# Kernel optimization log

Measured on AMD Instinct MI355X. Metric: run time of the kernel, lower is better.

## Reference

```python
import jax, jax.numpy as jnp
import numpy as np


def setup_inputs() -> dict:
    key = jax.random.key(0)
    k1, k2, k3 = jax.random.split(key, 3)
    B, D, F, P = 4096, 1024, 2048, 1024
    return {
        "x": jax.random.normal(k1, (B, D), dtype=jnp.float32),
        "features": jax.random.normal(k2, (F, D), dtype=jnp.float32),
        "prototypes": jax.random.normal(k3, (P, D), dtype=jnp.float32),
        "alpha": jnp.ones((1,), dtype=jnp.float32),
        "beta": jnp.ones((1,), dtype=jnp.float32),
        "theta": jnp.ones((1,), dtype=jnp.float32),
    }


def reference(x, features, prototypes, alpha, beta, theta):
    # Project each set ONCE (the original redundantly broadcasts first).
    xf = x @ features.T            # [B, F]
    pf = prototypes @ features.T   # [P, F]
    sx = jax.nn.sigmoid(xf)        # x_present [B, F]
    sp = jax.nn.sigmoid(pf)        # p_present [P, F]
    ax = xf * sx                   # [B, F]
    bp = pf * sp                   # [P, F]
    # common[b,p]        = sum_f xf*pf*sx*sp            = (xf*sx) @ (pf*sp)^T
    # x_distinct[b,p]    = sum_f xf*sx*(1-sp)           = rowsum(xf*sx) - (xf*sx) @ sp^T
    # p_distinct[b,p]    = sum_f pf*sp*(1-sx)           = rowsum(pf*sp) - sx @ (pf*sp)^T
    common = ax @ bp.T                                     # [B, P]
    x_distinctive = ax.sum(axis=1, keepdims=True) - ax @ sp.T  # [B, P]
    p_distinctive = bp.sum(axis=1)[None, :] - sx @ bp.T        # [B, P]
    return theta * common - alpha * x_distinctive - beta * p_distinctive
```

## Files before the change

### kernel.cpp

```cpp
#include <hip/hip_runtime.h>
#include <hip/hip_bf16.h>

typedef __bf16 bf16_t;
typedef bf16_t bf16x4 __attribute__((ext_vector_type(4)));
typedef bf16_t bf16x8 __attribute__((ext_vector_type(8)));
typedef float f32x4 __attribute__((ext_vector_type(4)));

#define AS1 __attribute__((address_space(1)))
#define AS3 __attribute__((address_space(3)))

__device__ __forceinline__ void gload_lds16(const void* g, void* l) {
    __builtin_amdgcn_global_load_lds((const AS1 void*)g, (AS3 void*)l, 16, 0, 0);
}
__device__ __forceinline__ void gload_lds4(const void* g, void* l) {
    __builtin_amdgcn_global_load_lds((const AS1 void*)g, (AS3 void*)l, 4, 0, 0);
}

__device__ __forceinline__ float sigmoidf_(float v) {
    return 1.0f / (1.0f + __expf(-v));
}

__global__ __launch_bounds__(256) void k_convert3(const float* __restrict__ x,
                                                  const float* __restrict__ pr,
                                                  const float* __restrict__ ft,
                                                  bf16_t* __restrict__ XPs,
                                                  bf16_t* __restrict__ F16s) {
    const int n4 = 7168 * 256;
    int i = blockIdx.x * 256 + threadIdx.x;
    const int stride = gridDim.x * 256;
    for (; i < n4; i += stride) {
        float4 v;
        long r;
        int c4;
        bf16_t* dst;
        long R;
        if (i < 1048576) {
            v = ((const float4*)x)[i];
            r = i >> 8; c4 = i & 255; dst = XPs; R = 5120;
        } else if (i < 1310720) {
            const int j = i - 1048576;
            v = ((const float4*)pr)[j];
            r = 4096 + (j >> 8); c4 = j & 255; dst = XPs; R = 5120;
        } else {
            const int j = i - 1310720;
            v = ((const float4*)ft)[j];
            r = j >> 8; c4 = j & 255; dst = F16s; R = 2048;
        }
        const int col = c4 << 2;
        const int kb = col >> 5;
        const int cw = col & 31;
        bf16x4 o;
        o[0] = (bf16_t)v.x; o[1] = (bf16_t)v.y; o[2] = (bf16_t)v.z; o[3] = (bf16_t)v.w;
        *(bf16x4*)(dst + ((long)kb * R + r) * 32 + cw) = o;
    }
}

__global__ __launch_bounds__(256) void k_foldrs(const float* __restrict__ rsPart,
                                                float* __restrict__ rsums) {
    const int r = blockIdx.x * 256 + threadIdx.x;
    float s = 0.f;
#pragma unroll
    for (int b = 0; b < 8; ++b) s += rsPart[b * 5120 + r];
    rsums[r] = s;
}

__global__ __launch_bounds__(256) void k_reduce4(const bf16_t* __restrict__ part,
                                                 const float* __restrict__ rsums,
                                                 const float* __restrict__ pa,
                                                 float* __restrict__ out) {
    const int idx = blockIdx.x * 256 + threadIdx.x;
    const int region = idx >> 13;
    const int widx = idx & 8191;
    const int wv = widx >> 10;
    const int chunk = (widx >> 6) & 15;
    const int ln = widx & 63;
    const int bx = region >> 2, by = region & 3;
    const int wm = wv >> 2, wn = wv & 3;
    const int fg = chunk >> 1, gp = chunk & 1;
    const int er = (ln >> 4) << 2, ec = ln & 15;
    const long off = (long)idx * 8;

    float sum[8] = {};
#pragma unroll
    for (int s = 0; s < 4; ++s) {
        bf16x8 v = *(const bf16x8*)(part + (long)s * 4194304 + off);
#pragma unroll
        for (int j = 0; j < 8; ++j) sum[j] += (float)v[j];
    }
    const int r0 = bx * 256 + wm * 128 + fg * 16 + er;
    const int c0 = by * 256 + wn * 64 + gp * 32 + ec;
    const float a = pa[0];
#pragma unroll
    for (int q = 0; q < 4; ++q) {
        const float ra = a * rsums[r0 + q];
#pragma unroll
        for (int gh = 0; gh < 2; ++gh) {
            const int c = c0 + gh * 16;
            out[(long)(r0 + q) * 1024 + c] = sum[gh * 4 + q] - ra - rsums[4096 + c];
        }
    }
}

__global__ __launch_bounds__(512, 2) void gemm2_8p(
    const bf16_t* __restrict__ A2s, const bf16_t* __restrict__ B2s,
    bf16_t* __restrict__ O1, long zstride) {
    __shared__ char lds[131072];
    const int tid = threadIdx.x;
    const int wave = tid >> 6, lane = tid & 63;
    const int wm = wave >> 2, wn = wave & 3;

    const int gx = gridDim.x, gy = gridDim.y;
    const int o = blockIdx.x + gx * (blockIdx.y + gy * blockIdx.z);
    const int cpx = (gx * gy * (int)gridDim.z) >> 3;
    const int v = (o & 7) * cpx + (o >> 3);
    const int bx = v % gx;
    const int rem = v / gx;
    const int by = rem % gy;
    const int bz = rem / gy;

    const long bm = (long)bx * 256, bn = (long)by * 256;
    const int kb32_0 = bz * 32;
    const char* Ab = (const char*)A2s;
    const char* Bb = (const char*)B2s;

    const int swzcb = ((lane >> 4) << 4) ^ (((lane >> 3) & 1) << 5);
    const int base_a = (wm * 128 + (lane & 15)) * 64 + swzcb;
    const int base_b = (wn * 64 + (lane & 15)) * 64 + swzcb;

    f32x4 acc[8][4] = {};

    auto STAGEC = [&](const char* gbase, int ldsoff) {
#pragma unroll
        for (int j = 0; j < 2; ++j) {
            const int oo = (j * 512 + tid) << 4;
            const int cb = (oo & 63) ^ (((oo >> 9) & 1) << 5);
            gload_lds16(gbase + (oo & ~63) + cb, lds + ldsoff + (oo & ~1023));
        }
    };

#define VM8 asm volatile("s_waitcnt vmcnt(8)" ::: "memory")
#define VM4 asm volatile("s_waitcnt vmcnt(4)" ::: "memory")
#define VM0 asm volatile("s_waitcnt vmcnt(0)" ::: "memory")

    auto PFETCH = [&](int pf) {
        const long kb = kb32_0 + pf;
        const int ps = pf & 3;
        STAGEC(Ab + (kb * 4096 + bm) * 64, ps * 16384);
        STAGEC(Bb + (kb * 1024 + bn) * 64, 65536 + ps * 16384);
    };

#define PHASE2(p, WAITSTMT, DOPF)                                               \
    do {                                                                        \
        WAITSTMT;                                                               \
        __builtin_amdgcn_s_barrier();                                           \
        __builtin_amdgcn_s_setprio(1);                                          \
        const int slot = (p) & 3;                                               \
        const char* sA = lds + slot * 16384;                                    \
        const char* sB = lds + 65536 + slot * 16384;                            \
        bf16x8 af[8];                                                           \
        bf16x8 bfr[4];                                                          \
        _Pragma("unroll") for (int f = 0; f < 8; ++f)                           \
            af[f] = *(const bf16x8*)(sA + base_a + f * 1024);                   \
        _Pragma("unroll") for (int g = 0; g < 4; ++g)                           \
            bfr[g] = *(const bf16x8*)(sB + base_b + g * 1024);                  \
        if (DOPF) PFETCH((p) + 3);                                              \
        _Pragma("unroll") for (int f = 0; f < 8; ++f)                           \
            _Pragma("unroll") for (int g = 0; g < 4; ++g)                       \
                acc[f][g] = __builtin_amdgcn_mfma_f32_16x16x32_bf16(            \
                    af[f], bfr[g], acc[f][g], 0, 0, 0);                         \
        __builtin_amdgcn_s_setprio(0);                                          \
    } while (0)

    const int NP = 32;
    PFETCH(0);
    PFETCH(1);
    PFETCH(2);

    for (int p = 0; p < NP - 3; ++p) PHASE2(p, VM8, 1);
    PHASE2(NP - 3, VM8, 0);
    PHASE2(NP - 2, VM4, 0);
    PHASE2(NP - 1, VM0, 0);

#undef PHASE2
#undef VM8
#undef VM4
#undef VM0

    bf16_t* Op = O1 + (long)bz * zstride + (long)(bx * 4 + by) * 65536 +
                 wave * 8192 + lane * 8;
#pragma unroll
    for (int fg = 0; fg < 8; ++fg)
#pragma unroll
        for (int gp = 0; gp < 2; ++gp) {
            bf16x8 w;
#pragma unroll
            for (int gh = 0; gh < 2; ++gh)
#pragma unroll
                for (int q = 0; q < 4; ++q)
                    w[gh * 4 + q] = (bf16_t)acc[fg][gp * 2 + gh][q];
            *(bf16x8*)(Op + (fg * 2 + gp) * 512) = w;
        }
}

__global__ __launch_bounds__(512, 2) void gemm1_160(
    const bf16_t* __restrict__ XPs, const bf16_t* __restrict__ F16s,
    bf16_t* __restrict__ A2s, bf16_t* __restrict__ B2s,
    float* __restrict__ rsPart,
    const float* __restrict__ pa, const float* __restrict__ pb,
    const float* __restrict__ pt) {
    __shared__ char lds[106496];
    const int tid = threadIdx.x;
    const int wave = tid >> 6, lane = tid & 63;
    const int wm = wave >> 2, wn = wave & 3;

    const int gx = gridDim.x, gy = gridDim.y;
    const int o = blockIdx.x + gx * blockIdx.y;
    const int cpx = (gx * gy) >> 3;
    const int v = (o & 7) * cpx + (o >> 3);
    const int bx = v % gx;
    const int by = v / gx;

    const long bm = (long)bx * 160, bn = (long)by * 256;
    const char* Ab = (const char*)XPs;
    const char* Bb = (const char*)F16s;

    const int swzcb = ((lane >> 4) << 4) ^ (((lane >> 3) & 1) << 5);
    const int base_a = (wm * 80 + (lane & 15)) * 64 + swzcb;
    const int base_b = (wn * 64 + (lane & 15)) * 64 + swzcb;

    f32x4 acc[5][4] = {};

#define VM8 asm volatile("s_waitcnt vmcnt(8)" ::: "memory")
#define VM4 asm volatile("s_waitcnt vmcnt(4)" ::: "memory")
#define VM0 asm volatile("s_waitcnt vmcnt(0)" ::: "memory")

    auto PFETCH = [&](int pf) {
        const int ps = pf & 3;
        const char* Ag = Ab + ((long)pf * 5120 + bm) * 64;
        const char* Bg = Bb + ((long)pf * 2048 + bn) * 64;
        {
            const int oo = tid << 4;
            const int cb = (oo & 63) ^ (((oo >> 9) & 1) << 5);
            gload_lds16(Ag + (oo & ~63) + cb, lds + ps * 10240 + (oo & ~1023));
        }
        {
            const int oo = 8192 + (tid << 2);
            const int cb = (oo & 63) ^ (((oo >> 9) & 1) << 5);
            gload_lds4(Ag + (oo & ~63) + cb, lds + ps * 10240 + 8192 + wave * 256);
        }
#pragma unroll
        for (int j = 0; j < 2; ++j) {
            const int oo = (j * 512 + tid) << 4;
            const int cb = (oo & 63) ^ (((oo >> 9) & 1) << 5);
            gload_lds16(Bg + (oo & ~63) + cb, lds + 40960 + ps * 16384 + (oo & ~1023));
        }
    };

#define PHASE1(p, WAITSTMT, DOPF)                                               \
    do {                                                                        \
        WAITSTMT;                                                               \
        __builtin_amdgcn_s_barrier();                                           \
        __builtin_amdgcn_s_setprio(1);                                          \
        const int slot = (p) & 3;                                               \
        const char* sA = lds + slot * 10240;                                    \
        const char* sB = lds + 40960 + slot * 16384;                            \
        bf16x8 af[5];                                                           \
        bf16x8 bfr[4];                                                          \
        _Pragma("unroll") for (int f = 0; f < 5; ++f)                           \
            af[f] = *(const bf16x8*)(sA + base_a + f * 1024);                   \
        _Pragma("unroll") for (int g = 0; g < 4; ++g)                           \
            bfr[g] = *(const bf16x8*)(sB + base_b + g * 1024);                  \
        if (DOPF) PFETCH((p) + 3);                                              \
        _Pragma("unroll") for (int f = 0; f < 5; ++f)                           \
            _Pragma("unroll") for (int g = 0; g < 4; ++g)                       \
                acc[f][g] = __builtin_amdgcn_mfma_f32_16x16x32_bf16(            \
                    bfr[g], af[f], acc[f][g], 0, 0, 0);                         \
        __builtin_amdgcn_s_setprio(0);                                          \
    } while (0)

    const int NP = 32;
    PFETCH(0);
    PFETCH(1);
    PFETCH(2);

    for (int p = 0; p < NP - 3; ++p) PHASE1(p, VM8, 1);
    PHASE1(NP - 3, VM8, 0);
    PHASE1(NP - 2, VM4, 0);
    PHASE1(NP - 1, VM0, 0);

#undef PHASE1
#undef VM8
#undef VM4
#undef VM0

    const float va = pa[0], vb = pb[0], vt = pt[0];
    const int lm = lane & 15;
    const int ln4 = (lane >> 4) << 2;
    const int kbbase = (int)(bn >> 5) + wn * 2;
    float rs[5];
#pragma unroll
    for (int f = 0; f < 5; ++f) rs[f] = 0.f;

#pragma unroll
    for (int mf = 0; mf < 5; ++mf) {
        const long grow = bm + wm * 80 + mf * 16 + lm;
        const bool isXf = (grow < 4096);
        const long rowidx = isXf ? grow : (grow - 4096);
        const long rowsz = isXf ? 4096 : 1024;
        bf16_t* base = isXf ? A2s : B2s;
#pragma unroll
        for (int g = 0; g < 4; ++g) {
            bf16x4 w0, w1;
            float rsl = 0.f;
#pragma unroll
            for (int q = 0; q < 4; ++q) {
                const float vv = acc[mf][g][q];
                const float s = sigmoidf_(vv);
                const float prod = vv * s;
                w0[q] = (bf16_t)(isXf ? prod : (vt * prod + va * s));
                w1[q] = (bf16_t)(isXf ? s : (vb * prod));
                rsl += isXf ? prod : vb * prod;
            }
            rs[mf] += rsl;
            const long kb = kbbase + (g >> 1);
            const int c0 = (g & 1) * 16 + ln4;
            *(bf16x4*)(base + (kb * rowsz + rowidx) * 32 + c0) = w0;
            *(bf16x4*)(base + ((kb + 64) * rowsz + rowidx) * 32 + c0) = w1;
        }
    }

    __syncthreads();
    float* lds_f = (float*)lds;
#pragma unroll
    for (int f = 0; f < 5; ++f) {
        float t = rs[f];
        t += __shfl_xor(t, 16);
        t += __shfl_xor(t, 32);
        if ((lane >> 4) == 0) lds_f[wn * 160 + wm * 80 + f * 16 + lm] = t;
    }
    __syncthreads();
    if (tid < 160) {
        const float s = lds_f[tid] + lds_f[160 + tid] + lds_f[320 + tid] + lds_f[480 + tid];
        rsPart[(long)by * 5120 + bm + tid] = s;
    }
}

extern "C" void kernel_launch(void* const* d_in, const int* in_sizes, int n_in,
                              void* d_out, int out_size, void* d_ws, size_t ws_size,
                              hipStream_t stream) {
    const float* x = (const float*)d_in[0];
    const float* feats = (const float*)d_in[1];
    const float* protos = (const float*)d_in[2];
    const float* pa = (const float*)d_in[3];
    const float* pb = (const float*)d_in[4];
    const float* pt = (const float*)d_in[5];
    float* out = (float*)d_out;

    constexpr long Bsz = 4096, D = 1024, F = 2048, P = 1024;

    bf16_t* XPs = (bf16_t*)d_ws;
    bf16_t* F16s = XPs + (Bsz + P) * D;
    bf16_t* A2s = F16s + F * D;
    bf16_t* B2s = A2s + Bsz * 2 * F;
    float* rsums = (float*)(B2s + P * 2 * F);
    bf16_t* part = (bf16_t*)(rsums + Bsz + P);
    float* rsPart = (float*)(part + 4L * Bsz * P);

    k_convert3<<<2048, 256, 0, stream>>>(x, protos, feats, XPs, F16s);

    gemm1_160<<<dim3(32, 8), 512, 0, stream>>>(XPs, F16s, A2s, B2s, rsPart, pa, pb, pt);

    k_foldrs<<<20, 256, 0, stream>>>(rsPart, rsums);

    gemm2_8p<<<dim3(Bsz / 256, P / 256, 4), 512, 0, stream>>>(
        A2s, B2s, part, (long)Bsz * P);

    k_reduce4<<<2048, 256, 0, stream>>>(part, rsums, pa, out);
}
```

Before: 87.31 us.

## Shrink GEMM tiles to 4-wave blocks with double-buffered LDS pipelines

Both GEMM kernels drop from 8-wave 512-thread blocks to 4-wave 256-thread blocks. GEMM1 now uses 128x128 tiles on a 40x16 grid, and GEMM2 uses 256x128 tiles on a 16x8x4 grid. The 4-slot, prefetch-3-ahead LDS ring becomes a 2-slot double buffer with an extra lgkmcnt wait and barrier before each prefetch. The row-sum fold and the reduce-kernel indexing are updated to match the new tiling. The goal is more blocks, better occupancy and load balance across CUs, and an end to the 160-row odd tile, at the cost of shallower prefetch and an extra barrier per k-step.

```diff
diff --git a/kernel.cpp b/kernel.cpp
--- a/kernel.cpp
+++ b/kernel.cpp
@@ -11,9 +11,6 @@
 
 __device__ __forceinline__ void gload_lds16(const void* g, void* l) {
     __builtin_amdgcn_global_load_lds((const AS1 void*)g, (AS3 void*)l, 16, 0, 0);
-}
-__device__ __forceinline__ void gload_lds4(const void* g, void* l) {
-    __builtin_amdgcn_global_load_lds((const AS1 void*)g, (AS3 void*)l, 4, 0, 0);
 }
 
 __device__ __forceinline__ float sigmoidf_(float v) {
@@ -60,7 +57,7 @@
     const int r = blockIdx.x * 256 + threadIdx.x;
     float s = 0.f;
 #pragma unroll
-    for (int b = 0; b < 8; ++b) s += rsPart[b * 5120 + r];
+    for (int b = 0; b < 16; ++b) s += rsPart[b * 5120 + r];
     rsums[r] = s;
 }
 
@@ -69,13 +66,13 @@
                                                  const float* __restrict__ pa,
                                                  float* __restrict__ out) {
     const int idx = blockIdx.x * 256 + threadIdx.x;
-    const int region = idx >> 13;
-    const int widx = idx & 8191;
+    const int region = idx >> 12;
+    const int widx = idx & 4095;
     const int wv = widx >> 10;
     const int chunk = (widx >> 6) & 15;
     const int ln = widx & 63;
-    const int bx = region >> 2, by = region & 3;
-    const int wm = wv >> 2, wn = wv & 3;
+    const int bx = region >> 3, by = region & 7;
+    const int wm = wv >> 1, wn = wv & 1;
     const int fg = chunk >> 1, gp = chunk & 1;
     const int er = (ln >> 4) << 2, ec = ln & 15;
     const long off = (long)idx * 8;
@@ -88,7 +85,7 @@
         for (int j = 0; j < 8; ++j) sum[j] += (float)v[j];
     }
     const int r0 = bx * 256 + wm * 128 + fg * 16 + er;
-    const int c0 = by * 256 + wn * 64 + gp * 32 + ec;
+    const int c0 = by * 128 + wn * 64 + gp * 32 + ec;
     const float a = pa[0];
 #pragma unroll
     for (int q = 0; q < 4; ++q) {
@@ -101,13 +98,14 @@
     }
 }
 
-__global__ __launch_bounds__(512, 2) void gemm2_8p(
+__global__ __launch_bounds__(256, 2) void gemm2_k(
     const bf16_t* __restrict__ A2s, const bf16_t* __restrict__ B2s,
     bf16_t* __restrict__ O1, long zstride) {
-    __shared__ char lds[131072];
+    __shared__ char lds[49152];
     const int tid = threadIdx.x;
     const int wave = tid >> 6, lane = tid & 63;
-    const int wm = wave >> 2, wn = wave & 3;
+    const int wm = wave >> 1, wn = wave & 1;
+    const int lm = lane & 15;
 
     const int gx = gridDim.x, gy = gridDim.y;
     const int o = blockIdx.x + gx * (blockIdx.y + gy * blockIdx.z);
@@ -118,35 +116,38 @@
     const int by = rem % gy;
     const int bz = rem / gy;
 
-    const long bm = (long)bx * 256, bn = (long)by * 256;
+    const long bm = (long)bx * 256, bn = (long)by * 128;
     const int kb32_0 = bz * 32;
     const char* Ab = (const char*)A2s;
     const char* Bb = (const char*)B2s;
 
     const int swzcb = ((lane >> 4) << 4) ^ (((lane >> 3) & 1) << 5);
-    const int base_a = (wm * 128 + (lane & 15)) * 64 + swzcb;
-    const int base_b = (wn * 64 + (lane & 15)) * 64 + swzcb;
+    const int base_a = (wm * 128 + lm) * 64 + swzcb;
+    const int base_b = (wn * 64 + lm) * 64 + swzcb;
 
     f32x4 acc[8][4] = {};
 
-    auto STAGEC = [&](const char* gbase, int ldsoff) {
-#pragma unroll
-        for (int j = 0; j < 2; ++j) {
-            const int oo = (j * 512 + tid) << 4;
-            const int cb = (oo & 63) ^ (((oo >> 9) & 1) << 5);
-            gload_lds16(gbase + (oo & ~63) + cb, lds + ldsoff + (oo & ~1023));
-        }
-    };
-
-#define VM8 asm volatile("s_waitcnt vmcnt(8)" ::: "memory")
-#define VM4 asm volatile("s_waitcnt vmcnt(4)" ::: "memory")
+#define VM6 asm volatile("s_waitcnt vmcnt(6)" ::: "memory")
 #define VM0 asm volatile("s_waitcnt vmcnt(0)" ::: "memory")
+#define LK0 asm volatile("s_waitcnt lgkmcnt(0)" ::: "memory")
 
     auto PFETCH = [&](int pf) {
         const long kb = kb32_0 + pf;
-        const int ps = pf & 3;
-        STAGEC(Ab + (kb * 4096 + bm) * 64, ps * 16384);
-        STAGEC(Bb + (kb * 1024 + bn) * 64, 65536 + ps * 16384);
+        const int ps = pf & 1;
+        const char* Ag = Ab + (kb * 4096 + bm) * 64;
+        const char* Bg = Bb + (kb * 1024 + bn) * 64;
+#pragma unroll
+        for (int j = 0; j < 4; ++j) {
+            const int oo = (j * 256 + tid) << 4;
+            const int cb = (oo & 63) ^ (((oo >> 9) & 1) << 5);
+            gload_lds16(Ag + (oo & ~63) + cb, lds + ps * 16384 + (oo & ~1023));
+        }
+#pragma unroll
+        for (int j = 0; j < 2; ++j) {
+            const int oo = (j * 256 + tid) << 4;
+            const int cb = (oo & 63) ^ (((oo >> 9) & 1) << 5);
+            gload_lds16(Bg + (oo & ~63) + cb, lds + 32768 + ps * 8192 + (oo & ~1023));
+        }
     };
 
 #define PHASE2(p, WAITSTMT, DOPF)                                               \
@@ -154,39 +155,40 @@
         WAITSTMT;                                                               \
         __builtin_amdgcn_s_barrier();                                           \
         __builtin_amdgcn_s_setprio(1);                                          \
-        const int slot = (p) & 3;                                               \
+        const int slot = (p) & 1;                                               \
         const char* sA = lds + slot * 16384;                                    \
-        const char* sB = lds + 65536 + slot * 16384;                            \
+        const char* sB = lds + 32768 + slot * 8192;                             \
         bf16x8 af[8];                                                           \
         bf16x8 bfr[4];                                                          \
         _Pragma("unroll") for (int f = 0; f < 8; ++f)                           \
             af[f] = *(const bf16x8*)(sA + base_a + f * 1024);                   \
         _Pragma("unroll") for (int g = 0; g < 4; ++g)                           \
             bfr[g] = *(const bf16x8*)(sB + base_b + g * 1024);                  \
-        if (DOPF) PFETCH((p) + 3);                                              \
         _Pragma("unroll") for (int f = 0; f < 8; ++f)                           \
             _Pragma("unroll") for (int g = 0; g < 4; ++g)                       \
                 acc[f][g] = __builtin_amdgcn_mfma_f32_16x16x32_bf16(            \
                     af[f], bfr[g], acc[f][g], 0, 0, 0);                         \
         __builtin_amdgcn_s_setprio(0);                                          \
+        if (DOPF) {                                                             \
+            LK0;                                                                \
+            __builtin_amdgcn_s_barrier();                                       \
+            PFETCH((p) + 2);                                                    \
+        }                                                                       \
     } while (0)
 
     const int NP = 32;
     PFETCH(0);
     PFETCH(1);
-    PFETCH(2);
-
-    for (int p = 0; p < NP - 3; ++p) PHASE2(p, VM8, 1);
-    PHASE2(NP - 3, VM8, 0);
-    PHASE2(NP - 2, VM4, 0);
+
+    for (int p = 0; p < NP - 1; ++p) PHASE2(p, VM6, (p < NP - 2));
     PHASE2(NP - 1, VM0, 0);
 
 #undef PHASE2
-#undef VM8
-#undef VM4
+#undef VM6
 #undef VM0
-
-    bf16_t* Op = O1 + (long)bz * zstride + (long)(bx * 4 + by) * 65536 +
+#undef LK0
+
+    bf16_t* Op = O1 + (long)bz * zstride + (long)(bx * 8 + by) * 32768 +
                  wave * 8192 + lane * 8;
 #pragma unroll
     for (int fg = 0; fg < 8; ++fg)
@@ -202,16 +204,17 @@
         }
 }
 
-__global__ __launch_bounds__(512, 2) void gemm1_160(
+__global__ __launch_bounds__(256, 2) void gemm1_k(
     const bf16_t* __restrict__ XPs, const bf16_t* __restrict__ F16s,
     bf16_t* __restrict__ A2s, bf16_t* __restrict__ B2s,
     float* __restrict__ rsPart,
     const float* __restrict__ pa, const float* __restrict__ pb,
     const float* __restrict__ pt) {
-    __shared__ char lds[106496];
+    __shared__ char lds[32768];
     const int tid = threadIdx.x;
     const int wave = tid >> 6, lane = tid & 63;
-    const int wm = wave >> 2, wn = wave & 3;
+    const int wm = wave >> 1, wn = wave & 1;
+    const int lm = lane & 15;
 
     const int gx = gridDim.x, gy = gridDim.y;
     const int o = blockIdx.x + gx * blockIdx.y;
@@ -220,39 +223,35 @@
     const int bx = v % gx;
     const int by = v / gx;
 
-    const long bm = (long)bx * 160, bn = (long)by * 256;
+    const long bm = (long)bx * 128, bn = (long)by * 128;
     const char* Ab = (const char*)XPs;
     const char* Bb = (const char*)F16s;
 
     const int swzcb = ((lane >> 4) << 4) ^ (((lane >> 3) & 1) << 5);
-    const int base_a = (wm * 80 + (lane & 15)) * 64 + swzcb;
-    const int base_b = (wn * 64 + (lane & 15)) * 64 + swzcb;
-
-    f32x4 acc[5][4] = {};
-
-#define VM8 asm volatile("s_waitcnt vmcnt(8)" ::: "memory")
+    const int base_a = (wm * 64 + lm) * 64 + swzcb;
+    const int base_b = (wn * 64 + lm) * 64 + swzcb;
+
+    f32x4 acc[4][4] = {};
+
 #define VM4 asm volatile("s_waitcnt vmcnt(4)" ::: "memory")
 #define VM0 asm volatile("s_waitcnt vmcnt(0)" ::: "memory")
+#define LK0 asm volatile("s_waitcnt lgkmcnt(0)" ::: "memory")
 
     auto PFETCH = [&](int pf) {
-        const int ps = pf & 3;
+        const int ps = pf & 1;
         const char* Ag = Ab + ((long)pf * 5120 + bm) * 64;
         const char* Bg = Bb + ((long)pf * 2048 + bn) * 64;
-        {
-            const int oo = tid << 4;
+#pragma unroll
+        for (int j = 0; j < 2; ++j) {
+            const int oo = (j * 256 + tid) << 4;
             const int cb = (oo & 63) ^ (((oo >> 9) & 1) << 5);
-            gload_lds16(Ag + (oo & ~63) + cb, lds + ps * 10240 + (oo & ~1023));
-        }
-        {
-            const int oo = 8192 + (tid << 2);
+            gload_lds16(Ag + (oo & ~63) + cb, lds + ps * 8192 + (oo & ~1023));
+        }
+#pragma unroll
+        for (int j = 0; j < 2; ++j) {
+            const int oo = (j * 256 + tid) << 4;
             const int cb = (oo & 63) ^ (((oo >> 9) & 1) << 5);
-            gload_lds4(Ag + (oo & ~63) + cb, lds + ps * 10240 + 8192 + wave * 256);
-        }
-#pragma unroll
-        for (int j = 0; j < 2; ++j) {
-            const int oo = (j * 512 + tid) << 4;
-            const int cb = (oo & 63) ^ (((oo >> 9) & 1) << 5);
-            gload_lds16(Bg + (oo & ~63) + cb, lds + 40960 + ps * 16384 + (oo & ~1023));
+            gload_lds16(Bg + (oo & ~63) + cb, lds + 16384 + ps * 8192 + (oo & ~1023));
         }
     };
 
@@ -261,49 +260,49 @@
         WAITSTMT;                                                               \
         __builtin_amdgcn_s_barrier();                                           \
         __builtin_amdgcn_s_setprio(1);                                          \
-        const int slot = (p) & 3;                                               \
-        const char* sA = lds + slot * 10240;                                    \
-        const char* sB = lds + 40960 + slot * 16384;                            \
-        bf16x8 af[5];                                                           \
+        const int slot = (p) & 1;                                               \
+        const char* sA = lds + slot * 8192;                                     \
+        const char* sB = lds + 16384 + slot * 8192;                             \
+        bf16x8 af[4];                                                           \
         bf16x8 bfr[4];                                                          \
-        _Pragma("unroll") for (int f = 0; f < 5; ++f)                           \
+        _Pragma("unroll") for (int f = 0; f < 4; ++f)                           \
             af[f] = *(const bf16x8*)(sA + base_a + f * 1024);                   \
         _Pragma("unroll") for (int g = 0; g < 4; ++g)                           \
             bfr[g] = *(const bf16x8*)(sB + base_b + g * 1024);                  \
-        if (DOPF) PFETCH((p) + 3);                                              \
-        _Pragma("unroll") for (int f = 0; f < 5; ++f)                           \
+        _Pragma("unroll") for (int f = 0; f < 4; ++f)                           \
             _Pragma("unroll") for (int g = 0; g < 4; ++g)                       \
                 acc[f][g] = __builtin_amdgcn_mfma_f32_16x16x32_bf16(            \
                     bfr[g], af[f], acc[f][g], 0, 0, 0);                         \
         __builtin_amdgcn_s_setprio(0);                                          \
+        if (DOPF) {                                                             \
+            LK0;                                                                \
+            __builtin_amdgcn_s_barrier();                                       \
+            PFETCH((p) + 2);                                                    \
+        }                                                                       \
     } while (0)
 
     const int NP = 32;
     PFETCH(0);
     PFETCH(1);
-    PFETCH(2);
-
-    for (int p = 0; p < NP - 3; ++p) PHASE1(p, VM8, 1);
-    PHASE1(NP - 3, VM8, 0);
-    PHASE1(NP - 2, VM4, 0);
+
+    for (int p = 0; p < NP - 1; ++p) PHASE1(p, VM4, (p < NP - 2));
     PHASE1(NP - 1, VM0, 0);
 
 #undef PHASE1
-#undef VM8
 #undef VM4
 #undef VM0
+#undef LK0
 
     const float va = pa[0], vb = pb[0], vt = pt[0];
-    const int lm = lane & 15;
     const int ln4 = (lane >> 4) << 2;
     const int kbbase = (int)(bn >> 5) + wn * 2;
-    float rs[5];
-#pragma unroll
-    for (int f = 0; f < 5; ++f) rs[f] = 0.f;
-
-#pragma unroll
-    for (int mf = 0; mf < 5; ++mf) {
-        const long grow = bm + wm * 80 + mf * 16 + lm;
+    float rs[4];
+#pragma unroll
+    for (int f = 0; f < 4; ++f) rs[f] = 0.f;
+
+#pragma unroll
+    for (int mf = 0; mf < 4; ++mf) {
+        const long grow = bm + wm * 64 + mf * 16 + lm;
         const bool isXf = (grow < 4096);
         const long rowidx = isXf ? grow : (grow - 4096);
         const long rowsz = isXf ? 4096 : 1024;
@@ -332,15 +331,15 @@
     __syncthreads();
     float* lds_f = (float*)lds;
 #pragma unroll
-    for (int f = 0; f < 5; ++f) {
+    for (int f = 0; f < 4; ++f) {
         float t = rs[f];
         t += __shfl_xor(t, 16);
         t += __shfl_xor(t, 32);
-        if ((lane >> 4) == 0) lds_f[wn * 160 + wm * 80 + f * 16 + lm] = t;
+        if ((lane >> 4) == 0) lds_f[wn * 128 + wm * 64 + f * 16 + lm] = t;
     }
     __syncthreads();
-    if (tid < 160) {
-        const float s = lds_f[tid] + lds_f[160 + tid] + lds_f[320 + tid] + lds_f[480 + tid];
+    if (tid < 128) {
+        const float s = lds_f[tid] + lds_f[128 + tid];
         rsPart[(long)by * 5120 + bm + tid] = s;
     }
 }
@@ -368,12 +367,11 @@
 
     k_convert3<<<2048, 256, 0, stream>>>(x, protos, feats, XPs, F16s);
 
-    gemm1_160<<<dim3(32, 8), 512, 0, stream>>>(XPs, F16s, A2s, B2s, rsPart, pa, pb, pt);
+    gemm1_k<<<dim3(40, 16), 256, 0, stream>>>(XPs, F16s, A2s, B2s, rsPart, pa, pb, pt);
 
     k_foldrs<<<20, 256, 0, stream>>>(rsPart, rsums);
 
-    gemm2_8p<<<dim3(Bsz / 256, P / 256, 4), 512, 0, stream>>>(
-        A2s, B2s, part, (long)Bsz * P);
+    gemm2_k<<<dim3(16, 8, 4), 256, 0, stream>>>(A2s, B2s, part, (long)Bsz * P);
 
     k_reduce4<<<2048, 256, 0, stream>>>(part, rsums, pa, out);
 }
```

After: 91.85 us. 1.05x slower.
